# Optimization experiments

Measured on AMD Instinct MI355X. Metric: run time of the kernel, lower is better.

## Reference

```python
import jax, jax.numpy as jnp
import numpy as np

EPS = 1e-6
NUM_HEADS = 32
HEAD_DIM = 128


def _rms_norm(x, w):
    # RMSNorm over last dim (head_dim)
    var = jnp.mean(x * x, axis=-1, keepdims=True)
    return x * jax.lax.rsqrt(var + EPS) * w


def _rotate_half(x):
    x1, x2 = jnp.split(x, 2, axis=-1)
    return jnp.concatenate([-x2, x1], axis=-1)


def _apply_rope(x, cos, sin):
    # x: [b, t, h, d]; cos/sin: [t, d] -> broadcast over batch and heads
    c = cos[None, :, None, :]
    s = sin[None, :, None, :]
    return x * c + _rotate_half(x) * s


def setup_inputs() -> dict:
    key = jax.random.key(0)
    ks = jax.random.split(key, 7)
    b, q_len, ctx_len, hidden = 4, 64, 4096, 4096
    total = ctx_len + q_len
    return {
        "hidden_states": jax.random.normal(ks[0], (b, q_len, hidden), jnp.float32),
        "target_hidden": jax.random.normal(ks[1], (b, ctx_len, hidden), jnp.float32),
        "cos": jax.random.uniform(ks[2], (total, HEAD_DIM), jnp.float32, -1.0, 1.0),
        "sin": jax.random.uniform(ks[3], (total, HEAD_DIM), jnp.float32, -1.0, 1.0),
        "Wqkv": jax.random.normal(ks[4], (hidden, 3 * hidden), jnp.float32) * 0.02,
        "Wo": jax.random.normal(ks[5], (hidden, hidden), jnp.float32) * 0.02,
        "q_norm_w": jnp.ones((HEAD_DIM,), jnp.float32),
    }


def reference(hidden_states, target_hidden, cos, sin, Wqkv, Wo, q_norm_w):
    b, q_len, hidden = hidden_states.shape
    ctx_len = target_hidden.shape[1]
    H, D = NUM_HEADS, HEAD_DIM

    # fused QKV projection; only the query slice is consumed (per source)
    qkv = jnp.einsum("bqh,hz->bqz", hidden_states, Wqkv)
    q = qkv[..., : H * D].reshape(b, q_len, H, D)

    # q_norm is applied twice in the source forward
    q = _rms_norm(_rms_norm(q, q_norm_w), q_norm_w)

    # KV built by concatenating raw target_hidden context with draft hidden states
    kv = jnp.concatenate([target_hidden, hidden_states], axis=1)  # [b, ctx+q, hidden]
    k = kv.reshape(b, ctx_len + q_len, H, D)
    v = k  # v = k view per source (rope applied only to k)

    # rotary: draft queries occupy positions ctx_len .. ctx_len+q_len-1
    q = _apply_rope(q, cos[ctx_len:], sin[ctx_len:])
    k = _apply_rope(k, cos, sin)

    # attention (full attention of draft queries over context + draft keys)
    scale = 1.0 / jnp.sqrt(jnp.asarray(D, q.dtype))
    scores = jnp.einsum("bqhd,bkhd->bhqk", q, k) * scale
    probs = jax.nn.softmax(scores, axis=-1)
    out = jnp.einsum("bhqk,bkhd->bqhd", probs, v)

    out = out.reshape(b, q_len, H * D)
    return jnp.einsum("bqh,ho->bqo", out, Wo)
```

## Files before the change

kernel.cpp:

```cpp
#include <hip/hip_runtime.h>

typedef __attribute__((ext_vector_type(8))) short bf16x8;
typedef __attribute__((ext_vector_type(4))) float f32x4;
typedef __attribute__((ext_vector_type(4))) short s16x4;

#define DEV __device__ __forceinline__

DEV short f2bf(float f) {
  union { float f; unsigned u; } v; v.f = f;
  unsigned r = v.u + 0x7fffu + ((v.u >> 16) & 1u);
  return (short)(r >> 16);
}

DEV int pk2(float a, float b) {
#if defined(__has_builtin) && __has_builtin(__builtin_amdgcn_cvt_pk_bf16_f32)
  auto v = __builtin_amdgcn_cvt_pk_bf16_f32(a, b);
  int r; __builtin_memcpy(&r, &v, 4); return r;
#else
  return (int)(unsigned short)f2bf(a) | ((int)(unsigned short)f2bf(b) << 16);
#endif
}

DEV void stage16(const short* g, short* lbase, int lane) {
#if defined(__has_builtin) && __has_builtin(__builtin_amdgcn_global_load_lds)
  (void)lane;
  __builtin_amdgcn_global_load_lds((const __attribute__((address_space(1))) void*)g,
                                   (__attribute__((address_space(3))) void*)lbase, 16, 0, 0);
#else
  *(bf16x8*)(lbase + lane * 8) = *(const bf16x8*)g;
#endif
}

__global__ __launch_bounds__(256) void transpose_to_bf16(
    const float* __restrict__ in, long ld, short* __restrict__ out, int K) {
  __shared__ short tile[64][66];
  long k0 = blockIdx.x * 64L, n0 = blockIdx.y * 64L;
  int t = threadIdx.x;
  {
    int kl = t >> 4, nl4 = (t & 15) * 4;
#pragma unroll
    for (int i = 0; i < 4; i++) {
      int k = kl + i * 16;
      float4 v = *(const float4*)(in + (k0 + k) * ld + n0 + nl4);
      int* dst = (int*)&tile[k][nl4];
      dst[0] = pk2(v.x, v.y);
      dst[1] = pk2(v.z, v.w);
    }
  }
  __syncthreads();
  {
    int nl = t >> 4, kl4 = (t & 15) * 4;
#pragma unroll
    for (int i = 0; i < 4; i++) {
      int n = nl + i * 16;
      s16x4 w;
      w.x = tile[kl4 + 0][n]; w.y = tile[kl4 + 1][n];
      w.z = tile[kl4 + 2][n]; w.w = tile[kl4 + 3][n];
      *(s16x4*)(out + (n0 + n) * (long)K + k0 + kl4) = w;
    }
  }
}

__global__ __launch_bounds__(256) void cast_f32_bf16(
    const float* __restrict__ in, short* __restrict__ out, int n8) {
  int i = blockIdx.x * 256 + threadIdx.x;
  if (i >= n8) return;
  float4 a = *(const float4*)(in + (long)i * 8);
  float4 b = *(const float4*)(in + (long)i * 8 + 4);
  union { bf16x8 v; int w[4]; } r;
  r.w[0] = pk2(a.x, a.y); r.w[1] = pk2(a.z, a.w);
  r.w[2] = pk2(b.x, b.y); r.w[3] = pk2(b.z, b.w);
  *(bf16x8*)(out + (long)i * 8) = r.v;
}

__global__ __launch_bounds__(512) void gemm_dma(
    const short* __restrict__ A, const short* __restrict__ Bt,
    float* __restrict__ Cp, int N, int K, int Kc) {
  __shared__ short As[32 * 512];
  __shared__ short Bs[8 * 512];
  int t = threadIdx.x;
  int lane = t & 63, wave = t >> 6;
  int quad = lane >> 4, m16 = lane & 15;
  long n0 = blockIdx.x * 64L;
  int z = blockIdx.y;
  f32x4 acc[2][4] = {};
  int kbeg = z * Kc, kend = kbeg + Kc;

  for (int k0 = kbeg; k0 < kend; k0 += 64) {
    __syncthreads();
#pragma unroll
    for (int i = 0; i < 2; i++)
#pragma unroll
      for (int s = 0; s < 2; s++) {
        int row = (2 * wave + i) * 16 + m16;
        const short* g = A + (long)row * K + k0 + (s * 4 + quad) * 8;
        stage16(g, &As[(4 * wave + 2 * i + s) * 512], lane);
      }
    {
      int nt = wave >> 1, s = wave & 1;
      long row = n0 + nt * 16 + m16;
      const short* g = Bt + row * (long)K + k0 + (s * 4 + quad) * 8;
      stage16(g, &Bs[wave * 512], lane);
    }
    __syncthreads();
#pragma unroll
    for (int s = 0; s < 2; s++) {
      bf16x8 a0 = *(bf16x8*)&As[(4 * wave + s) * 512 + lane * 8];
      bf16x8 a1 = *(bf16x8*)&As[(4 * wave + 2 + s) * 512 + lane * 8];
#pragma unroll
      for (int nt = 0; nt < 4; nt++) {
        bf16x8 b = *(bf16x8*)&Bs[(nt * 2 + s) * 512 + lane * 8];
        acc[0][nt] = __builtin_amdgcn_mfma_f32_16x16x32_bf16(a0, b, acc[0][nt], 0, 0, 0);
        acc[1][nt] = __builtin_amdgcn_mfma_f32_16x16x32_bf16(a1, b, acc[1][nt], 0, 0, 0);
      }
    }
  }
  float* C = Cp + (long)z * 256 * N;
#pragma unroll
  for (int i = 0; i < 2; i++)
#pragma unroll
    for (int nt = 0; nt < 4; nt++)
#pragma unroll
      for (int rg = 0; rg < 4; rg++) {
        long m = (2 * wave + i) * 16 + quad * 4 + rg;
        C[m * (long)N + n0 + nt * 16 + m16] = acc[i][nt][rg];
      }
}

__global__ __launch_bounds__(256) void reduce8(
    const float* __restrict__ p, float* __restrict__ out, long n4, long stride) {
  long i = (blockIdx.x * 256L + threadIdx.x);
  if (i >= n4) return;
  float4 r = *(const float4*)(p + i * 4);
#pragma unroll
  for (int z = 1; z < 8; z++) {
    float4 a = *(const float4*)(p + z * stride + i * 4);
    r.x += a.x; r.y += a.y; r.z += a.z; r.w += a.w;
  }
  *(float4*)(out + i * 4) = r;
}

__global__ __launch_bounds__(256) void q_norm_rope(
    const float* __restrict__ qtmp, const float* __restrict__ qw,
    const float* __restrict__ cosp, const float* __restrict__ sinp,
    short* __restrict__ qr) {
  int wid = blockIdx.x * 4 + (threadIdx.x >> 6);
  int lane = threadIdx.x & 63;
  int rrow = wid >> 5, h = wid & 31;
  long base = (long)rrow * 4096 + h * 128;
  const long STR = 256L * 4096;
  float x1 = 0.f, x2 = 0.f;
#pragma unroll
  for (int z = 0; z < 8; z++) {
    x1 += qtmp[z * STR + base + lane];
    x2 += qtmp[z * STR + base + 64 + lane];
  }
  float w1 = qw[lane], w2 = qw[64 + lane];
  float ss = x1 * x1 + x2 * x2;
#pragma unroll
  for (int m = 1; m < 64; m <<= 1) ss += __shfl_xor(ss, m, 64);
  float rs = rsqrtf(ss * (1.0f / 128.0f) + 1e-6f);
  float y1 = x1 * rs * w1, y2 = x2 * rs * w2;
  float ss2 = y1 * y1 + y2 * y2;
#pragma unroll
  for (int m = 1; m < 64; m <<= 1) ss2 += __shfl_xor(ss2, m, 64);
  float rs2 = rsqrtf(ss2 * (1.0f / 128.0f) + 1e-6f);
  float z1 = y1 * rs2 * w1, z2 = y2 * rs2 * w2;
  long cpos = (long)(4096 + (rrow & 63)) * 128;
  float c1 = cosp[cpos + lane], c2 = cosp[cpos + 64 + lane];
  float s1 = sinp[cpos + lane], s2 = sinp[cpos + 64 + lane];
  const float scale = 0.08838834764831845f;
  float o1 = (z1 * c1 - z2 * s1) * scale;
  float o2 = (z2 * c2 + z1 * s2) * scale;
  qr[base + lane] = f2bf(o1);
  qr[base + 64 + lane] = f2bf(o2);
}

#define ATT_SPLIT 13
#define ATT_LKV 320
#define ATT_TILES 5

__global__ __launch_bounds__(256) void attn_kernel(
    const short* __restrict__ qr, const float* __restrict__ th,
    const float* __restrict__ hs, const float* __restrict__ cosp,
    const float* __restrict__ sinp, float* __restrict__ part,
    float* __restrict__ mstat, float* __restrict__ lstat) {
  __shared__ short Ks[64 * 136];
  __shared__ short Vt[128 * 80];
  __shared__ short Ps[64 * 72];
  int bh = blockIdx.x, split = blockIdx.y;
  int b = bh >> 5, h = bh & 31;
  int t = threadIdx.x;
  int wave = t >> 6, lane = t & 63, quad = lane >> 4, m16 = lane & 15;

  bf16x8 aq[4];
  {
    const short* qrow = qr + (long)(b * 64 + wave * 16 + m16) * 4096 + h * 128;
#pragma unroll
    for (int s = 0; s < 4; s++) aq[s] = *(const bf16x8*)(qrow + s * 32 + quad * 8);
  }
  float mi[4] = {-INFINITY, -INFINITY, -INFINITY, -INFINITY};
  float li[4] = {0.f, 0.f, 0.f, 0.f};
  f32x4 oacc[8] = {};

  int srow = t >> 2;
  int sc = t & 3;
  int colw = srow ^ (sc * 16);

  for (int tile = 0; tile < ATT_TILES; tile++) {
    int l0 = split * ATT_LKV + tile * 64;
    __syncthreads();
    {
      int lg = l0 + srow;
      const float* kvrow = (lg < 4096)
          ? th + ((long)b * 4096 + lg) * 4096 + h * 128
          : hs + ((long)b * 64 + (lg - 4096)) * 4096 + h * 128;
      const float* crow = cosp + (long)lg * 128;
      const float* srw = sinp + (long)lg * 128;
#pragma unroll
      for (int i = 0; i < 2; i++) {
        int c = sc + 4 * i;
        int d1 = c * 8, d2 = d1 + 64;
        alignas(16) float xa[8], xb[8], cA[8], sA[8], cB[8], sB[8];
        *(float4*)&xa[0] = *(const float4*)(kvrow + d1);
        *(float4*)&xa[4] = *(const float4*)(kvrow + d1 + 4);
        *(float4*)&xb[0] = *(const float4*)(kvrow + d2);
        *(float4*)&xb[4] = *(const float4*)(kvrow + d2 + 4);
        *(float4*)&cA[0] = *(const float4*)(crow + d1);
        *(float4*)&cA[4] = *(const float4*)(crow + d1 + 4);
        *(float4*)&cB[0] = *(const float4*)(crow + d2);
        *(float4*)&cB[4] = *(const float4*)(crow + d2 + 4);
        *(float4*)&sA[0] = *(const float4*)(srw + d1);
        *(float4*)&sA[4] = *(const float4*)(srw + d1 + 4);
        *(float4*)&sB[0] = *(const float4*)(srw + d2);
        *(float4*)&sB[4] = *(const float4*)(srw + d2 + 4);
        union { bf16x8 v; int w[4]; } K1, K2;
#pragma unroll
        for (int jj = 0; jj < 4; jj++) {
          int j0 = 2 * jj, j1 = 2 * jj + 1;
          K1.w[jj] = pk2(xa[j0] * cA[j0] - xb[j0] * sA[j0],
                         xa[j1] * cA[j1] - xb[j1] * sA[j1]);
          K2.w[jj] = pk2(xb[j0] * cB[j0] + xa[j0] * sB[j0],
                         xb[j1] * cB[j1] + xa[j1] * sB[j1]);
        }
        *(bf16x8*)&Ks[srow * 136 + d1] = K1.v;
        *(bf16x8*)&Ks[srow * 136 + d2] = K2.v;
#pragma unroll
        for (int jj = 0; jj < 4; jj++) {
          int p1 = pk2(xa[2 * jj], xa[2 * jj + 1]);
          int p2 = pk2(xb[2 * jj], xb[2 * jj + 1]);
          Vt[(d1 + 2 * jj) * 80 + colw] = (short)(p1 & 0xffff);
          Vt[(d1 + 2 * jj + 1) * 80 + colw] = (short)((unsigned)p1 >> 16);
          Vt[(d2 + 2 * jj) * 80 + colw] = (short)(p2 & 0xffff);
          Vt[(d2 + 2 * jj + 1) * 80 + colw] = (short)((unsigned)p2 >> 16);
        }
      }
    }
    __syncthreads();

    f32x4 sacc[4] = {};
#pragma unroll
    for (int s = 0; s < 4; s++)
#pragma unroll
      for (int nt = 0; nt < 4; nt++) {
        bf16x8 bk = *(const bf16x8*)&Ks[(nt * 16 + m16) * 136 + s * 32 + quad * 8];
        sacc[nt] = __builtin_amdgcn_mfma_f32_16x16x32_bf16(aq[s], bk, sacc[nt], 0, 0, 0);
      }

    float mnew[4], alpha[4];
#pragma unroll
    for (int rg = 0; rg < 4; rg++) {
      float mx = fmaxf(fmaxf(sacc[0][rg], sacc[1][rg]), fmaxf(sacc[2][rg], sacc[3][rg]));
#pragma unroll
      for (int msk = 1; msk < 16; msk <<= 1) mx = fmaxf(mx, __shfl_xor(mx, msk, 16));
      mnew[rg] = fmaxf(mi[rg], mx);
      alpha[rg] = __expf(mi[rg] - mnew[rg]);
      mi[rg] = mnew[rg];
    }
#pragma unroll
    for (int rg = 0; rg < 4; rg++) {
      float rs = 0.f;
#pragma unroll
      for (int nt = 0; nt < 4; nt++) {
        float p = __expf(sacc[nt][rg] - mnew[rg]);
        rs += p;
        Ps[(wave * 16 + quad * 4 + rg) * 72 + nt * 16 + m16] = f2bf(p);
      }
#pragma unroll
      for (int msk = 1; msk < 16; msk <<= 1) rs += __shfl_xor(rs, msk, 16);
      li[rg] = li[rg] * alpha[rg] + rs;
    }
#pragma unroll
    for (int nt = 0; nt < 8; nt++) {
      f32x4 o = oacc[nt];
      o[0] *= alpha[0]; o[1] *= alpha[1]; o[2] *= alpha[2]; o[3] *= alpha[3];
      oacc[nt] = o;
    }

    bf16x8 ap[2];
#pragma unroll
    for (int s = 0; s < 2; s++)
      ap[s] = *(const bf16x8*)&Ps[(wave * 16 + m16) * 72 + s * 32 + quad * 8];
#pragma unroll
    for (int s = 0; s < 2; s++)
#pragma unroll
      for (int nt = 0; nt < 8; nt++) {
        int d16 = nt * 16 + m16;
        int scd = (d16 >> 3) & 3;
        int cb = (s * 32 + quad * 8) ^ (scd * 16);
        bf16x8 bv = *(const bf16x8*)&Vt[d16 * 80 + cb];
        oacc[nt] = __builtin_amdgcn_mfma_f32_16x16x32_bf16(ap[s], bv, oacc[nt], 0, 0, 0);
      }
  }

  long pbase = (long)(bh * ATT_SPLIT + split) * 64;
#pragma unroll
  for (int nt = 0; nt < 8; nt++)
#pragma unroll
    for (int rg = 0; rg < 4; rg++)
      part[(pbase + wave * 16 + quad * 4 + rg) * 128 + nt * 16 + m16] = oacc[nt][rg];
  if (m16 == 0)
#pragma unroll
    for (int rg = 0; rg < 4; rg++) {
      mstat[pbase + wave * 16 + quad * 4 + rg] = mi[rg];
      lstat[pbase + wave * 16 + quad * 4 + rg] = li[rg];
    }
}

__global__ __launch_bounds__(128) void attn_merge(
    const float* __restrict__ part, const float* __restrict__ mstat,
    const float* __restrict__ lstat, short* __restrict__ attn) {
  int idx = blockIdx.x;
  int bh = idx >> 6, q = idx & 63;
  int d = threadIdx.x;
  float mstar = -INFINITY;
#pragma unroll
  for (int s = 0; s < ATT_SPLIT; s++)
    mstar = fmaxf(mstar, mstat[((long)bh * ATT_SPLIT + s) * 64 + q]);
  float denom = 0.f, o = 0.f;
#pragma unroll
  for (int s = 0; s < ATT_SPLIT; s++) {
    long sq = ((long)bh * ATT_SPLIT + s) * 64 + q;
    float w = __expf(mstat[sq] - mstar);
    denom += w * lstat[sq];
    o += w * part[sq * 128 + d];
  }
  int b = bh >> 5, h = bh & 31;
  attn[(long)(b * 64 + q) * 4096 + h * 128 + d] = f2bf(o / denom);
}

extern "C" void kernel_launch(void* const* d_in, const int* in_sizes, int n_in,
                              void* d_out, int out_size, void* d_ws, size_t ws_size,
                              hipStream_t stream) {
  const float* hs = (const float*)d_in[0];
  const float* th = (const float*)d_in[1];
  const float* cosp = (const float*)d_in[2];
  const float* sinp = (const float*)d_in[3];
  const float* wqkv = (const float*)d_in[4];
  const float* wo = (const float*)d_in[5];
  const float* qw = (const float*)d_in[6];
  float* out = (float*)d_out;

  char* ws = (char*)d_ws;
  short* WT   = (short*)ws;
  short* hsb  = (short*)(ws + (32L << 20));
  float* qtmp = (float*)(ws + (34L << 20));
  short* qrb  = (short*)(ws + (66L << 20));
  short* attnb= (short*)(ws + (68L << 20));
  float* part = (float*)(ws + (70L << 20));
  float* mstat= (float*)(ws + (125L << 20));
  float* lstat= (float*)(ws + (126L << 20));
  float* otmp = (float*)(ws + (127L << 20));

  transpose_to_bf16<<<dim3(64, 64), 256, 0, stream>>>(wqkv, 12288, WT, 4096);
  cast_f32_bf16<<<512, 256, 0, stream>>>(hs, hsb, 131072);
  gemm_dma<<<dim3(64, 8), 512, 0, stream>>>(hsb, WT, qtmp, 4096, 4096, 512);
  q_norm_rope<<<2048, 256, 0, stream>>>(qtmp, qw, cosp, sinp, qrb);
  attn_kernel<<<dim3(128, ATT_SPLIT), 256, 0, stream>>>(qrb, th, hs, cosp, sinp,
                                                        part, mstat, lstat);
  attn_merge<<<128 * 64, 128, 0, stream>>>(part, mstat, lstat, attnb);
  transpose_to_bf16<<<dim3(64, 64), 256, 0, stream>>>(wo, 4096, WT, 4096);
  gemm_dma<<<dim3(64, 8), 512, 0, stream>>>(attnb, WT, otmp, 4096, 4096, 512);
  reduce8<<<1024, 256, 0, stream>>>(otmp, out, 262144, 1048576);
}
```

Baseline: 633.9 us.

## Prefetch raw KV tiles into LDS, merge weight prep, atomically reduce output GEMM

The attention kernel now stages the next tile's raw fp32 K/V rows into a swizzled LDS buffer through async global-to-LDS loads while the current tile runs MFMA, and it uses fewer, longer splits (7×10 tiles). Both weight transposes are merged into one launch. The output GEMM accumulates split-K partials with atomic adds into the output, which is zeroed by the cast kernel, so the reduce8 pass and its partial buffer go away. The cost is 32 KB of extra LDS per block, which may lower occupancy, plus atomic contention and a nondeterministic summation order.

```diff
diff --git a/kernel.cpp b/kernel.cpp
--- a/kernel.cpp
+++ b/kernel.cpp
@@ -31,9 +31,24 @@
 #endif
 }
 
-__global__ __launch_bounds__(256) void transpose_to_bf16(
-    const float* __restrict__ in, long ld, short* __restrict__ out, int K) {
+DEV void stage16f(const float* g, float* lbase, int lane) {
+#if defined(__has_builtin) && __has_builtin(__builtin_amdgcn_global_load_lds)
+  (void)lane;
+  __builtin_amdgcn_global_load_lds((const __attribute__((address_space(1))) void*)g,
+                                   (__attribute__((address_space(3))) void*)lbase, 16, 0, 0);
+#else
+  *(float4*)(lbase + lane * 4) = *(const float4*)g;
+#endif
+}
+
+__global__ __launch_bounds__(256) void prep_w(
+    const float* __restrict__ wqkv, const float* __restrict__ wo,
+    short* __restrict__ out) {
   __shared__ short tile[64][66];
+  int z = blockIdx.z;
+  const float* in = z ? wo : wqkv;
+  long ld = z ? 4096 : 12288;
+  short* o = out + (long)z * 16777216L;
   long k0 = blockIdx.x * 64L, n0 = blockIdx.y * 64L;
   int t = threadIdx.x;
   {
@@ -56,13 +71,14 @@
       s16x4 w;
       w.x = tile[kl4 + 0][n]; w.y = tile[kl4 + 1][n];
       w.z = tile[kl4 + 2][n]; w.w = tile[kl4 + 3][n];
-      *(s16x4*)(out + (n0 + n) * (long)K + k0 + kl4) = w;
+      *(s16x4*)(o + (n0 + n) * 4096L + k0 + kl4) = w;
     }
   }
 }
 
 __global__ __launch_bounds__(256) void cast_f32_bf16(
-    const float* __restrict__ in, short* __restrict__ out, int n8) {
+    const float* __restrict__ in, short* __restrict__ out, int n8,
+    float* __restrict__ zbuf) {
   int i = blockIdx.x * 256 + threadIdx.x;
   if (i >= n8) return;
   float4 a = *(const float4*)(in + (long)i * 8);
@@ -71,6 +87,9 @@
   r.w[0] = pk2(a.x, a.y); r.w[1] = pk2(a.z, a.w);
   r.w[2] = pk2(b.x, b.y); r.w[3] = pk2(b.z, b.w);
   *(bf16x8*)(out + (long)i * 8) = r.v;
+  float4 z4 = make_float4(0.f, 0.f, 0.f, 0.f);
+  *(float4*)(zbuf + (long)i * 8) = z4;
+  *(float4*)(zbuf + (long)i * 8 + 4) = z4;
 }
 
 __global__ __launch_bounds__(512) void gemm_dma(
@@ -127,17 +146,57 @@
       }
 }
 
-__global__ __launch_bounds__(256) void reduce8(
-    const float* __restrict__ p, float* __restrict__ out, long n4, long stride) {
-  long i = (blockIdx.x * 256L + threadIdx.x);
-  if (i >= n4) return;
-  float4 r = *(const float4*)(p + i * 4);
-#pragma unroll
-  for (int z = 1; z < 8; z++) {
-    float4 a = *(const float4*)(p + z * stride + i * 4);
-    r.x += a.x; r.y += a.y; r.z += a.z; r.w += a.w;
-  }
-  *(float4*)(out + i * 4) = r;
+__global__ __launch_bounds__(512) void gemm_dma_atomic(
+    const short* __restrict__ A, const short* __restrict__ Bt,
+    float* __restrict__ C, int N, int K, int Kc) {
+  __shared__ short As[32 * 512];
+  __shared__ short Bs[8 * 512];
+  int t = threadIdx.x;
+  int lane = t & 63, wave = t >> 6;
+  int quad = lane >> 4, m16 = lane & 15;
+  long n0 = blockIdx.x * 64L;
+  int z = blockIdx.y;
+  f32x4 acc[2][4] = {};
+  int kbeg = z * Kc, kend = kbeg + Kc;
+
+  for (int k0 = kbeg; k0 < kend; k0 += 64) {
+    __syncthreads();
+#pragma unroll
+    for (int i = 0; i < 2; i++)
+#pragma unroll
+      for (int s = 0; s < 2; s++) {
+        int row = (2 * wave + i) * 16 + m16;
+        const short* g = A + (long)row * K + k0 + (s * 4 + quad) * 8;
+        stage16(g, &As[(4 * wave + 2 * i + s) * 512], lane);
+      }
+    {
+      int nt = wave >> 1, s = wave & 1;
+      long row = n0 + nt * 16 + m16;
+      const short* g = Bt + row * (long)K + k0 + (s * 4 + quad) * 8;
+      stage16(g, &Bs[wave * 512], lane);
+    }
+    __syncthreads();
+#pragma unroll
+    for (int s = 0; s < 2; s++) {
+      bf16x8 a0 = *(bf16x8*)&As[(4 * wave + s) * 512 + lane * 8];
+      bf16x8 a1 = *(bf16x8*)&As[(4 * wave + 2 + s) * 512 + lane * 8];
+#pragma unroll
+      for (int nt = 0; nt < 4; nt++) {
+        bf16x8 b = *(bf16x8*)&Bs[(nt * 2 + s) * 512 + lane * 8];
+        acc[0][nt] = __builtin_amdgcn_mfma_f32_16x16x32_bf16(a0, b, acc[0][nt], 0, 0, 0);
+        acc[1][nt] = __builtin_amdgcn_mfma_f32_16x16x32_bf16(a1, b, acc[1][nt], 0, 0, 0);
+      }
+    }
+  }
+#pragma unroll
+  for (int i = 0; i < 2; i++)
+#pragma unroll
+    for (int nt = 0; nt < 4; nt++)
+#pragma unroll
+      for (int rg = 0; rg < 4; rg++) {
+        long m = (2 * wave + i) * 16 + quad * 4 + rg;
+        unsafeAtomicAdd(&C[m * (long)N + n0 + nt * 16 + m16], acc[i][nt][rg]);
+      }
 }
 
 __global__ __launch_bounds__(256) void q_norm_rope(
@@ -176,9 +235,8 @@
   qr[base + 64 + lane] = f2bf(o2);
 }
 
-#define ATT_SPLIT 13
-#define ATT_LKV 320
-#define ATT_TILES 5
+#define ATT_SPLIT 7
+#define ATT_TILES 10
 
 __global__ __launch_bounds__(256) void attn_kernel(
     const short* __restrict__ qr, const float* __restrict__ th,
@@ -188,11 +246,15 @@
   __shared__ short Ks[64 * 136];
   __shared__ short Vt[128 * 80];
   __shared__ short Ps[64 * 72];
+  __shared__ float Xraw[64 * 128];
   int bh = blockIdx.x, split = blockIdx.y;
   int b = bh >> 5, h = bh & 31;
   int t = threadIdx.x;
   int wave = t >> 6, lane = t & 63, quad = lane >> 4, m16 = lane & 15;
 
+  int tile0 = split * ATT_TILES;
+  int ntiles = (65 - tile0 < ATT_TILES) ? (65 - tile0) : ATT_TILES;
+
   bf16x8 aq[4];
   {
     const short* qrow = qr + (long)(b * 64 + wave * 16 + m16) * 4096 + h * 128;
@@ -207,25 +269,39 @@
   int sc = t & 3;
   int colw = srow ^ (sc * 16);
 
-  for (int tile = 0; tile < ATT_TILES; tile++) {
-    int l0 = split * ATT_LKV + tile * 64;
+  {
+    int tl = tile0;
+#pragma unroll
+    for (int j = 0; j < 8; j++) {
+      int r = (wave * 8 + j) * 2 + (lane >> 5);
+      int lgn = tl * 64 + r;
+      int cs = lane & 31;
+      int fo = (cs ^ (r & 7)) << 2;
+      const float* src = (lgn < 4096)
+          ? th + ((long)b * 4096 + lgn) * 4096 + h * 128 + fo
+          : hs + ((long)b * 64 + (lgn - 4096)) * 4096 + h * 128 + fo;
+      stage16f(src, &Xraw[(wave * 8 + j) * 256], lane);
+    }
+  }
+
+  for (int tt = 0; tt < ntiles; tt++) {
+    int lg = (tile0 + tt) * 64 + srow;
     __syncthreads();
     {
-      int lg = l0 + srow;
-      const float* kvrow = (lg < 4096)
-          ? th + ((long)b * 4096 + lg) * 4096 + h * 128
-          : hs + ((long)b * 64 + (lg - 4096)) * 4096 + h * 128;
       const float* crow = cosp + (long)lg * 128;
       const float* srw = sinp + (long)lg * 128;
+      const float* xrow = Xraw + srow * 128;
+      int sx = srow & 7;
 #pragma unroll
       for (int i = 0; i < 2; i++) {
         int c = sc + 4 * i;
         int d1 = c * 8, d2 = d1 + 64;
+        int c0 = c * 2;
         alignas(16) float xa[8], xb[8], cA[8], sA[8], cB[8], sB[8];
-        *(float4*)&xa[0] = *(const float4*)(kvrow + d1);
-        *(float4*)&xa[4] = *(const float4*)(kvrow + d1 + 4);
-        *(float4*)&xb[0] = *(const float4*)(kvrow + d2);
-        *(float4*)&xb[4] = *(const float4*)(kvrow + d2 + 4);
+        *(float4*)&xa[0] = *(const float4*)(xrow + ((c0 ^ sx) << 2));
+        *(float4*)&xa[4] = *(const float4*)(xrow + (((c0 + 1) ^ sx) << 2));
+        *(float4*)&xb[0] = *(const float4*)(xrow + (((c0 + 16) ^ sx) << 2));
+        *(float4*)&xb[4] = *(const float4*)(xrow + (((c0 + 17) ^ sx) << 2));
         *(float4*)&cA[0] = *(const float4*)(crow + d1);
         *(float4*)&cA[4] = *(const float4*)(crow + d1 + 4);
         *(float4*)&cB[0] = *(const float4*)(crow + d2);
@@ -257,6 +333,21 @@
       }
     }
     __syncthreads();
+
+    if (tt + 1 < ntiles) {
+      int tl = tile0 + tt + 1;
+#pragma unroll
+      for (int j = 0; j < 8; j++) {
+        int r = (wave * 8 + j) * 2 + (lane >> 5);
+        int lgn = tl * 64 + r;
+        int cs = lane & 31;
+        int fo = (cs ^ (r & 7)) << 2;
+        const float* src = (lgn < 4096)
+            ? th + ((long)b * 4096 + lgn) * 4096 + h * 128 + fo
+            : hs + ((long)b * 64 + (lgn - 4096)) * 4096 + h * 128 + fo;
+        stage16f(src, &Xraw[(wave * 8 + j) * 256], lane);
+      }
+    }
 
     f32x4 sacc[4] = {};
 #pragma unroll
@@ -363,23 +454,21 @@
 
   char* ws = (char*)d_ws;
   short* WT   = (short*)ws;
-  short* hsb  = (short*)(ws + (32L << 20));
-  float* qtmp = (float*)(ws + (34L << 20));
-  short* qrb  = (short*)(ws + (66L << 20));
-  short* attnb= (short*)(ws + (68L << 20));
-  float* part = (float*)(ws + (70L << 20));
-  float* mstat= (float*)(ws + (125L << 20));
-  float* lstat= (float*)(ws + (126L << 20));
-  float* otmp = (float*)(ws + (127L << 20));
-
-  transpose_to_bf16<<<dim3(64, 64), 256, 0, stream>>>(wqkv, 12288, WT, 4096);
-  cast_f32_bf16<<<512, 256, 0, stream>>>(hs, hsb, 131072);
+  short* hsb  = (short*)(ws + (64L << 20));
+  float* qtmp = (float*)(ws + (66L << 20));
+  short* qrb  = (short*)(ws + (98L << 20));
+  short* attnb= (short*)(ws + (100L << 20));
+  float* part = (float*)(ws + (102L << 20));
+  float* mstat= (float*)(ws + (131L << 20));
+  float* lstat= (float*)(ws + (132L << 20));
+
+  prep_w<<<dim3(64, 64, 2), 256, 0, stream>>>(wqkv, wo, WT);
+  cast_f32_bf16<<<512, 256, 0, stream>>>(hs, hsb, 131072, out);
   gemm_dma<<<dim3(64, 8), 512, 0, stream>>>(hsb, WT, qtmp, 4096, 4096, 512);
   q_norm_rope<<<2048, 256, 0, stream>>>(qtmp, qw, cosp, sinp, qrb);
   attn_kernel<<<dim3(128, ATT_SPLIT), 256, 0, stream>>>(qrb, th, hs, cosp, sinp,
                                                         part, mstat, lstat);
   attn_merge<<<128 * 64, 128, 0, stream>>>(part, mstat, lstat, attnb);
-  transpose_to_bf16<<<dim3(64, 64), 256, 0, stream>>>(wo, 4096, WT, 4096);
-  gemm_dma<<<dim3(64, 8), 512, 0, stream>>>(attnb, WT, otmp, 4096, 4096, 512);
-  reduce8<<<1024, 256, 0, stream>>>(otmp, out, 262144, 1048576);
-}
+  gemm_dma_atomic<<<dim3(64, 8), 512, 0, stream>>>(attnb, WT + 16777216L, out,
+                                                   4096, 4096, 512);
+}
```

After: 631.5 us. No clear change (-0.4%).
